# Optimization experiments

Measured on AMD Instinct MI355X. Metric: run time of the kernel, lower is better.

## Reference

```python
import jax, jax.numpy as jnp
import numpy as np

N, E = 50000, 500000
IN_C, HID, OUT_C, HEADS, NL = 128, 16, 16, 8, 4
EPS = 1e-5
NEG_SLOPE = 0.2


def _gatv2(x, src, dst, Wl, Wr, att, bias, concat):
    # GATv2Conv (PyG semantics, eval mode): lin_l on source, lin_r on target,
    # e = a . LeakyReLU(xl[src] + xr[dst]); segment softmax over dst; scatter-sum.
    n = x.shape[0]
    H, C = att.shape
    xl = (x @ Wl).reshape(n, H, C)
    xr = (x @ Wr).reshape(n, H, C)
    e = jax.nn.leaky_relu(xl[src] + xr[dst], NEG_SLOPE)          # [E', H, C]
    logit = jnp.einsum('ehc,hc->eh', e, att)                      # [E', H]
    mx = jax.lax.stop_gradient(jax.ops.segment_max(logit, dst, num_segments=n))
    a = jnp.exp(logit - mx[dst])
    denom = jax.ops.segment_sum(a, dst, num_segments=n)
    alpha = a / denom[dst]                                        # [E', H]
    out = jax.ops.segment_sum(xl[src] * alpha[..., None], dst, num_segments=n)
    out = out.reshape(n, H * C) if concat else out.mean(axis=1)
    return out + bias


def _bn_eval(x, g, b, m, v):
    return (x - m) * jax.lax.rsqrt(v + EPS) * g + b


def setup_inputs() -> dict:
    key = jax.random.key(0)
    ks = jax.random.split(key, 32)
    d = {}
    d['x'] = jax.random.normal(ks[0], (N, IN_C), dtype=jnp.float32)
    d['edge_index'] = jax.random.randint(ks[1], (2, E), 0, N, dtype=jnp.int64)
    HC = HID * HEADS  # 128
    dims_in = [IN_C, HC, HC, HC]
    dims_h = [HEADS, HEADS, HEADS, 1]
    dims_c = [HID, HID, HID, OUT_C]
    ki = 2
    for i in range(NL):
        fan = dims_in[i]
        s = 1.0 / np.sqrt(fan)
        d[f'W{i}l'] = jax.random.uniform(ks[ki], (fan, dims_h[i] * dims_c[i]), minval=-s, maxval=s, dtype=jnp.float32); ki += 1
        d[f'W{i}r'] = jax.random.uniform(ks[ki], (fan, dims_h[i] * dims_c[i]), minval=-s, maxval=s, dtype=jnp.float32); ki += 1
        d[f'a{i}'] = jax.random.normal(ks[ki], (dims_h[i], dims_c[i]), dtype=jnp.float32) * 0.1; ki += 1
        out_dim = dims_h[i] * dims_c[i] if i < NL - 1 else dims_c[i]
        d[f'b{i}'] = jnp.zeros((out_dim,), dtype=jnp.float32)
    for i in range(NL - 1):
        d[f'g{i}'] = jnp.ones((HC,), dtype=jnp.float32) + 0.1 * jax.random.normal(ks[ki], (HC,), dtype=jnp.float32); ki += 1
        d[f'be{i}'] = 0.1 * jax.random.normal(ks[ki], (HC,), dtype=jnp.float32); ki += 1
        d[f'm{i}'] = 0.1 * jax.random.normal(ks[ki], (HC,), dtype=jnp.float32); ki += 1
        d[f'v{i}'] = jnp.ones((HC,), dtype=jnp.float32)
    return d


def reference(x, edge_index, W0l, W0r, a0, b0, W1l, W1r, a1, b1, W2l, W2r, a2, b2, W3l, W3r, a3, b3, g0, be0, m0, v0, g1, be1, m1, v1, g2, be2, m2, v2):
    n = x.shape[0]
    loop = jnp.arange(n, dtype=edge_index.dtype)
    src = jnp.concatenate([edge_index[0], loop])  # add_self_loops=True (PyG default)
    dst = jnp.concatenate([edge_index[1], loop])
    Ws = [(W0l, W0r, a0, b0), (W1l, W1r, a1, b1), (W2l, W2r, a2, b2), (W3l, W3r, a3, b3)]
    bns = [(g0, be0, m0, v0), (g1, be1, m1, v1), (g2, be2, m2, v2)]
    h = x
    for i in range(NL):
        Wl, Wr, att, bias = Ws[i]
        h = _gatv2(h, src, dst, Wl, Wr, att, bias, concat=(i < NL - 1))
        if i < NL - 1:
            g, b, m, v = bns[i]
            h = jax.nn.elu(_bn_eval(h, g, b, m, v))
    return h
```

## Files before the change

### kernel.cpp

```cpp
#include <hip/hip_runtime.h>
#include <hip/hip_fp16.h>
#include <math.h>

static constexpr float BN_EPS = 1e-5f;
static constexpr float NEG = 0.2f;

typedef float f32x4 __attribute__((ext_vector_type(4)));
typedef _Float16 h16x2 __attribute__((ext_vector_type(2)));
typedef _Float16 h16x8 __attribute__((ext_vector_type(8)));


__global__ __launch_bounds__(256) void hist_pack(
    const int* __restrict__ ei, int E, int n, int* __restrict__ cnt,
    const float* __restrict__ W0l, const float* __restrict__ W0r,
    const float* __restrict__ W1l, const float* __restrict__ W1r,
    const float* __restrict__ W2l, const float* __restrict__ W2r,
    const float* __restrict__ W3l, const float* __restrict__ W3r,
    __half* __restrict__ pk0, __half* __restrict__ pk1,
    __half* __restrict__ pk2, __half* __restrict__ pk3,
    const float* __restrict__ b0, const float* __restrict__ b1,
    const float* __restrict__ b2,
    const float* __restrict__ g0, const float* __restrict__ g1,
    const float* __restrict__ g2,
    const float* __restrict__ be0, const float* __restrict__ be1,
    const float* __restrict__ be2,
    const float* __restrict__ m0, const float* __restrict__ m1,
    const float* __restrict__ m2,
    const float* __restrict__ v0, const float* __restrict__ v1,
    const float* __restrict__ v2,
    float* __restrict__ bnA, float* __restrict__ bnB) {
    int b = blockIdx.x;
    if (b < 200) {
        if (threadIdx.x >= 64) return;
        const float *Wl, *Wr;
        __half* packed;
        int tile, NTT, M;
        if (b < 192) {
            int layer = b >> 6;
            tile = b & 63;
            NTT = 16; M = 128;
            Wl = (layer == 0) ? W0l : (layer == 1) ? W1l : W2l;
            Wr = (layer == 0) ? W0r : (layer == 1) ? W1r : W2r;
            packed = (layer == 0) ? pk0 : (layer == 1) ? pk1 : pk2;
        } else {
            tile = b - 192;
            NTT = 2; M = 16;
            Wl = W3l; Wr = W3r; packed = pk3;
        }
        int NT = NTT >> 1;
        int gnt = tile % NTT;
        int kt = tile / NTT;
        int l = threadIdx.x;
        const float* W = (gnt < NT) ? Wl : Wr;
        int col = (gnt % NT) * 16 + (l & 15);
        int krow = kt * 32 + ((l >> 4) << 3);
        size_t base = (size_t)tile * 512 + (size_t)l * 8;
#pragma unroll
        for (int j = 0; j < 8; j++)
            packed[base + j] = __float2half(W[(size_t)(krow + j) * M + col]);
    } else if (b == 200) {
        for (int t = threadIdx.x; t < 384; t += 256) {
            int layer = t >> 7;
            int c = t & 127;
            const float* gg = (layer == 0) ? g0 : (layer == 1) ? g1 : g2;
            const float* ee = (layer == 0) ? be0 : (layer == 1) ? be1 : be2;
            const float* mm = (layer == 0) ? m0 : (layer == 1) ? m1 : m2;
            const float* vv = (layer == 0) ? v0 : (layer == 1) ? v1 : v2;
            const float* bb = (layer == 0) ? b0 : (layer == 1) ? b1 : b2;
            float A = gg[c] * rsqrtf(vv[c] + BN_EPS);
            bnA[t] = A;
            bnB[t] = fmaf(bb[c] - mm[c], A, ee[c]);
        }
    } else {
        int e = (b - 201) * 256 + threadIdx.x;
        int ET = E + n;
        if (e >= ET) return;
        int d = (e < E) ? ei[E + e] : (e - E);
        atomicAdd(&cnt[d], 1);
    }
}


__device__ __forceinline__ void scan_block_body256(
    const int* __restrict__ cnt, int* __restrict__ rowptr,
    int* __restrict__ bsums, int n, int bid, int* s) {
    int t = threadIdx.x;
    int base = bid * 1024 + t * 4;
    int v0 = 0, v1 = 0, v2 = 0, v3 = 0;
    if (base + 3 < n) {
        v0 = cnt[base];     v1 = cnt[base + 1];
        v2 = cnt[base + 2]; v3 = cnt[base + 3];
    } else {
        if (base < n)     v0 = cnt[base];
        if (base + 1 < n) v1 = cnt[base + 1];
        if (base + 2 < n) v2 = cnt[base + 2];
        if (base + 3 < n) v3 = cnt[base + 3];
    }
    int p1 = v0 + v1, p2 = p1 + v2, p3 = p2 + v3;
    s[t] = p3;
    __syncthreads();
    for (int d = 1; d < 256; d <<= 1) {
        int tt = (t >= d) ? s[t - d] : 0;
        __syncthreads();
        s[t] += tt;
        __syncthreads();
    }
    int ex = s[t] - p3;
    if (base < n)     rowptr[base + 1] = ex + v0;
    if (base + 1 < n) rowptr[base + 2] = ex + p1;
    if (base + 2 < n) rowptr[base + 3] = ex + p2;
    if (base + 3 < n) rowptr[base + 4] = ex + p3;
    if (t == 255) bsums[bid] = s[255];
}

__global__ __launch_bounds__(1024) void scan_add2(
    int* __restrict__ rowptr, const int* __restrict__ bsums, int n, int nb,
    int* __restrict__ fill) {
    __shared__ int sex;
    if (threadIdx.x < 64) {
        int L = threadIdx.x;
        int v = (L < nb) ? bsums[L] : 0;
#pragma unroll
        for (int d = 1; d < 64; d <<= 1) {
            int t = __shfl_up(v, d);
            if (L >= d) v += t;
        }
        int ex = __shfl_up(v, 1);
        if (L == 0) ex = 0;
        if (L == (int)blockIdx.x) sex = ex;
    }
    __syncthreads();
    int i = blockIdx.x * 1024 + threadIdx.x;
    if (i < n) {
        int fin = rowptr[i + 1] + sex;
        rowptr[i + 1] = fin;
        if (i + 1 < n) fill[i + 1] = fin;
    }
    if (i == 0) { rowptr[0] = 0; fill[0] = 0; }
}

__global__ void scatter_kernel(const int* __restrict__ ei, int E, int n,
                               int* __restrict__ fill, int* __restrict__ col) {
    int e = blockIdx.x * blockDim.x + threadIdx.x;
    int ET = E + n;
    if (e >= ET) return;
    int s, d;
    if (e < E) { s = ei[e]; d = ei[E + e]; } else { s = e - E; d = s; }
    int pos = atomicAdd(&fill[d], 1);
    col[pos] = s;
}


template <bool FIRST>
__device__ __forceinline__ void gemm_body(
    const __half* __restrict__ xh, const float* __restrict__ xf,
    const __half* __restrict__ packed,
    __half* __restrict__ Y1, __half* __restrict__ Y2, int n, int bid,
    _Float16* sA) {
    const int t = threadIdx.x;
    const int row0 = bid * 64;

    for (int c = t; c < 1024; c += 256) {
        int row = c >> 4;
        int off = (c & 15) * 8;
        int gr = row0 + row;
        if (gr >= n) gr = n - 1;
        if (FIRST) {
            float4 v0 = *(const float4*)&xf[(size_t)gr * 128 + off];
            float4 v1 = *(const float4*)&xf[(size_t)gr * 128 + off + 4];
            h16x8 h = {(_Float16)v0.x, (_Float16)v0.y, (_Float16)v0.z, (_Float16)v0.w,
                       (_Float16)v1.x, (_Float16)v1.y, (_Float16)v1.z, (_Float16)v1.w};
            *(h16x8*)&sA[row * 136 + off] = h;
        } else {
            *(h16x8*)&sA[row * 136 + off] = *(const h16x8*)&xh[(size_t)gr * 128 + off];
        }
    }
    __syncthreads();

    const int lane = t & 63;
    const int s = t >> 6;
    const int lr = lane & 15;
    const int kq = (lane >> 4) * 8;

    h16x8 af[4][4];
#pragma unroll
    for (int rt = 0; rt < 4; rt++)
#pragma unroll
        for (int kt = 0; kt < 4; kt++)
            af[rt][kt] = *(const h16x8*)&sA[(rt * 16 + lr) * 136 + kt * 32 + kq];

    f32x4 acc[4][4];
#pragma unroll
    for (int a = 0; a < 4; a++)
#pragma unroll
        for (int b = 0; b < 4; b++) acc[a][b] = (f32x4){0.f, 0.f, 0.f, 0.f};

#pragma unroll
    for (int kt = 0; kt < 4; kt++) {
#pragma unroll
        for (int ntl = 0; ntl < 4; ntl++) {
            int nt = s * 4 + ntl;
            h16x8 b = *(const h16x8*)&packed[((size_t)(kt * 16 + nt)) * 512 + lane * 8];
#pragma unroll
            for (int rt = 0; rt < 4; rt++)
                acc[ntl][rt] = __builtin_amdgcn_mfma_f32_16x16x32_f16(b, af[rt][kt], acc[ntl][rt], 0, 0, 0);
        }
    }

    __half* Y = (s < 2) ? Y1 : Y2;
    const int colh = (s & 1) * 64;
    const int rq = (lane >> 4) * 4;
#pragma unroll
    for (int rt = 0; rt < 4; rt++) {
        int row = row0 + rt * 16 + lr;
        if (row >= n) continue;
#pragma unroll
        for (int ntl = 0; ntl < 4; ntl++) {
            int c0 = colh + ntl * 16 + rq;
            ushort4 o = make_ushort4(
                __half_as_ushort(__float2half(acc[ntl][rt][0])),
                __half_as_ushort(__float2half(acc[ntl][rt][1])),
                __half_as_ushort(__float2half(acc[ntl][rt][2])),
                __half_as_ushort(__float2half(acc[ntl][rt][3])));
            *(ushort4*)&Y[(size_t)row * 128 + c0] = o;
        }
    }
}

__global__ __launch_bounds__(256) void gemm_h_big2(
    const __half* __restrict__ xh, const __half* __restrict__ packed,
    __half* __restrict__ Y1, __half* __restrict__ Y2, int n) {
    __shared__ __align__(16) char smem[64 * 136 * 2];
    gemm_body<false>(xh, nullptr, packed, Y1, Y2, n, blockIdx.x, (_Float16*)smem);
}

__global__ __launch_bounds__(256) void scanblk_gemm0(
    const int* __restrict__ cnt, int* __restrict__ rowptr,
    int* __restrict__ bsums, int n, int nscan,
    const float* __restrict__ xf, const __half* __restrict__ packed,
    __half* __restrict__ Y1, __half* __restrict__ Y2) {
    __shared__ __align__(16) char smem[64 * 136 * 2];
    int b = blockIdx.x;
    if (b < nscan) {
        scan_block_body256(cnt, rowptr, bsums, n, b, (int*)smem);
    } else {
        gemm_body<true>(nullptr, xf, packed, Y1, Y2, n, b - nscan,
                        (_Float16*)smem);
    }
}


__global__ __launch_bounds__(256) void gemm_h_small(
    const __half* __restrict__ xh, const __half* __restrict__ packed,
    float* __restrict__ Y1, float* __restrict__ Y2, int n) {
    int lane = threadIdx.x & 63;
    int wv = blockIdx.x * 4 + (threadIdx.x >> 6);
    int row0 = wv * 16;
    if (row0 >= n) return;
    int r = row0 + (lane & 15);
    int rl = (r >= n) ? (n - 1) : r;
    int kq = (lane >> 4) * 8;

    h16x8 af[4];
#pragma unroll
    for (int kt = 0; kt < 4; kt++)
        af[kt] = *(const h16x8*)&xh[(size_t)rl * 128 + kt * 32 + kq];

    f32x4 acc[2];
    acc[0] = (f32x4){0.f, 0.f, 0.f, 0.f};
    acc[1] = (f32x4){0.f, 0.f, 0.f, 0.f};

#pragma unroll
    for (int kt = 0; kt < 4; kt++) {
#pragma unroll
        for (int nt = 0; nt < 2; nt++) {
            h16x8 b = *(const h16x8*)&packed[((size_t)(kt * 2 + nt)) * 512 + lane * 8];
            acc[nt] = __builtin_amdgcn_mfma_f32_16x16x32_f16(b, af[kt], acc[nt], 0, 0, 0);
        }
    }

    if (r < n) {
        int rq = (lane >> 4) * 4;
#pragma unroll
        for (int nt = 0; nt < 2; nt++) {
            float* Y = (nt == 0) ? Y1 : Y2;
            *(float4*)&Y[(size_t)r * 16 + rq] =
                make_float4(acc[nt][0], acc[nt][1], acc[nt][2], acc[nt][3]);
        }
    }
}


__device__ __forceinline__ float dot8_h(const h16x2* lp, const h16x2* ap) {
#if __has_builtin(__builtin_amdgcn_fdot2)
    float part = __builtin_amdgcn_fdot2(lp[0], ap[0], 0.f, false);
    part = __builtin_amdgcn_fdot2(lp[1], ap[1], part, false);
    part = __builtin_amdgcn_fdot2(lp[2], ap[2], part, false);
    return __builtin_amdgcn_fdot2(lp[3], ap[3], part, false);
#else
    float part = 0.f;
#pragma unroll
    for (int i = 0; i < 4; i++)
        part += (float)lp[i].x * (float)ap[i].x + (float)lp[i].y * (float)ap[i].y;
    return part;
#endif
}

__global__ __launch_bounds__(256) void agg_h(
    const __half* __restrict__ xl, const __half* __restrict__ xr,
    const int* __restrict__ rowptr, const int* __restrict__ col,
    const float* __restrict__ att,
    const float* __restrict__ bnA, const float* __restrict__ bnB,
    __half* __restrict__ oh, int n) {
    int v = (blockIdx.x * blockDim.x + threadIdx.x) >> 4;
    if (v >= n) return;
    int L = threadIdx.x & 15;
    int ch = L * 8;

    int beg = rowptr[v];
    int end = rowptr[v + 1];
    int cb = beg;
    int cidx = (cb + L < end) ? col[cb + L] : v;

    h16x8 rx = *(const h16x8*)&xr[((size_t)v << 7) + ch];
    float4 av0 = *(const float4*)&att[ch];
    float4 av1 = *(const float4*)&att[ch + 4];
    h16x2 a[4] = {{(_Float16)av0.x, (_Float16)av0.y},
                  {(_Float16)av0.z, (_Float16)av0.w},
                  {(_Float16)av1.x, (_Float16)av1.y},
                  {(_Float16)av1.z, (_Float16)av1.w}};
    const h16x8 neg8 = {(_Float16)NEG, (_Float16)NEG, (_Float16)NEG, (_Float16)NEG,
                        (_Float16)NEG, (_Float16)NEG, (_Float16)NEG, (_Float16)NEG};

    float lrun = 0.f;
    float acc[8] = {0.f, 0.f, 0.f, 0.f, 0.f, 0.f, 0.f, 0.f};

    auto proc = [&](h16x8 hv, bool ok) {
        h16x8 s = hv + rx;
        h16x8 l = __builtin_elementwise_max(s, s * neg8);
        const h16x2* lp = (const h16x2*)&l;
        float part = dot8_h(lp, a);
        part += __shfl_xor(part, 1);
        float p = ok ? __expf(part) : 0.f;
        lrun += p;
        const _Float16* hp = (const _Float16*)&hv;
#pragma unroll
        for (int k = 0; k < 8; k++) acc[k] = fmaf(p, (float)hp[k], acc[k]);
    };

    while (true) {
        int ce = min(end, cb + 16);
        for (int e = cb; e < ce; e += 4) {
            int off = e - cb;
            h16x8 hv[4];
#pragma unroll
            for (int j = 0; j < 4; j++) {
                int u = __shfl(cidx, off + j, 16);
                hv[j] = *(const h16x8*)&xl[((size_t)u << 7) + ch];
            }
#pragma unroll
            for (int j = 0; j < 4; j++) proc(hv[j], e + j < end);
        }
        cb += 16;
        if (cb >= end) break;
        cidx = (cb + L < end) ? col[cb + L] : v;
    }

    float inv = 1.0f / lrun;
    float4 A0 = *(const float4*)&bnA[ch];
    float4 A1 = *(const float4*)&bnA[ch + 4];
    float4 B0 = *(const float4*)&bnB[ch];
    float4 B1 = *(const float4*)&bnB[ch + 4];
    float Av[8] = {A0.x, A0.y, A0.z, A0.w, A1.x, A1.y, A1.z, A1.w};
    float Bv[8] = {B0.x, B0.y, B0.z, B0.w, B1.x, B1.y, B1.z, B1.w};
    h16x8 outv;
#pragma unroll
    for (int k = 0; k < 8; k++) {
        float o = fmaf(acc[k], inv * Av[k], Bv[k]);
        o = o > 0.f ? o : expm1f(o);
        outv[k] = (_Float16)o;
    }
    *(h16x8*)&oh[((size_t)v << 7) + ch] = outv;
}


__global__ __launch_bounds__(256) void agg_f(
    const float* __restrict__ xl, const float* __restrict__ xr,
    const int* __restrict__ rowptr, const int* __restrict__ col,
    const float* __restrict__ att, const float* __restrict__ bias,
    float* __restrict__ out, int n) {
    int v = (blockIdx.x * blockDim.x + threadIdx.x) >> 2;
    if (v >= n) return;
    int L = threadIdx.x & 3;
    int ch = 4 * L;

    int beg = rowptr[v];
    int end = rowptr[v + 1];
    int cb = beg;
    int cidx = (cb + L < end) ? col[cb + L] : v;

    float4 xrv = *(const float4*)&xr[((size_t)v << 4) + ch];
    float4 av = *(const float4*)&att[ch];

    float lrun = 0.f;
    float4 acc = make_float4(0.f, 0.f, 0.f, 0.f);

    while (true) {
        float4 xv[4];
#pragma unroll
        for (int j = 0; j < 4; j++) {
            int u = __shfl(cidx, j, 4);
            xv[j] = *(const float4*)&xl[((size_t)u << 4) + ch];
        }
#pragma unroll
        for (int j = 0; j < 4; j++) {
            bool ok = (cb + j < end);
            float s0 = xv[j].x + xrv.x; s0 = s0 > 0.f ? s0 : NEG * s0;
            float s1 = xv[j].y + xrv.y; s1 = s1 > 0.f ? s1 : NEG * s1;
            float s2 = xv[j].z + xrv.z; s2 = s2 > 0.f ? s2 : NEG * s2;
            float s3 = xv[j].w + xrv.w; s3 = s3 > 0.f ? s3 : NEG * s3;
            float part = fmaf(s0, av.x, fmaf(s1, av.y, fmaf(s2, av.z, s3 * av.w)));
            part += __shfl_xor(part, 1);
            part += __shfl_xor(part, 2);
            float p = ok ? __expf(part) : 0.f;
            lrun += p;
            acc.x = fmaf(p, xv[j].x, acc.x);
            acc.y = fmaf(p, xv[j].y, acc.y);
            acc.z = fmaf(p, xv[j].z, acc.z);
            acc.w = fmaf(p, xv[j].w, acc.w);
        }
        cb += 4;
        if (cb >= end) break;
        cidx = (cb + L < end) ? col[cb + L] : v;
    }

    float inv = 1.0f / lrun;
    float4 b4 = *(const float4*)&bias[ch];
    *(float4*)&out[((size_t)v << 4) + ch] =
        make_float4(fmaf(acc.x, inv, b4.x), fmaf(acc.y, inv, b4.y),
                    fmaf(acc.z, inv, b4.z), fmaf(acc.w, inv, b4.w));
}


extern "C" void kernel_launch(void* const* d_in, const int* in_sizes, int n_in,
                              void* d_out, int out_size, void* d_ws, size_t ws_size,
                              hipStream_t stream) {
    const float* x = (const float*)d_in[0];
    const int* ei = (const int*)d_in[1];
    const float* Wl[4] = {(const float*)d_in[2], (const float*)d_in[6],
                          (const float*)d_in[10], (const float*)d_in[14]};
    const float* Wr[4] = {(const float*)d_in[3], (const float*)d_in[7],
                          (const float*)d_in[11], (const float*)d_in[15]};
    const float* att[4] = {(const float*)d_in[4], (const float*)d_in[8],
                           (const float*)d_in[12], (const float*)d_in[16]};
    const float* bias[4] = {(const float*)d_in[5], (const float*)d_in[9],
                            (const float*)d_in[13], (const float*)d_in[17]};
    const float* g[3] = {(const float*)d_in[18], (const float*)d_in[22], (const float*)d_in[26]};
    const float* be[3] = {(const float*)d_in[19], (const float*)d_in[23], (const float*)d_in[27]};
    const float* bm[3] = {(const float*)d_in[20], (const float*)d_in[24], (const float*)d_in[28]};
    const float* bv[3] = {(const float*)d_in[21], (const float*)d_in[25], (const float*)d_in[29]};

    const int n = in_sizes[0] / 128;
    const int E = in_sizes[1] / 2;
    const int ET = E + n;

    char* p = (char*)d_ws;
    __half* xh = (__half*)p;           p += (size_t)n * 128 * 2;
    __half* xlh = (__half*)p;          p += (size_t)n * 128 * 2;
    __half* xrh = (__half*)p;          p += (size_t)n * 128 * 2;
    float* xl3 = (float*)p;            p += (size_t)n * 16 * 4;
    float* xr3 = (float*)p;            p += (size_t)n * 16 * 4;
    int* rowptr = (int*)p;            p += (size_t)(n + 4) * 4;
    int* cnt = (int*)p;               p += (size_t)n * 4;
    int* fill = (int*)p;              p += (size_t)n * 4;
    int* col = (int*)p;               p += (size_t)ET * 4;
    int* bsums = (int*)p;             p += 256;
    __half* pk[4];
    for (int i = 0; i < 3; i++) { pk[i] = (__half*)p; p += 4 * 16 * 512 * 2; }
    pk[3] = (__half*)p;               p += 4 * 2 * 512 * 2;
    float* bnA = (float*)p;           p += 384 * 4;
    float* bnB = (float*)p;           p += 384 * 4;

    (void)hipMemsetAsync(cnt, 0, (size_t)n * 4, stream);

    const int tb = 256;
    const int histBlocks = (ET + tb - 1) / tb;
    hist_pack<<<201 + histBlocks, tb, 0, stream>>>(
        ei, E, n, cnt,
        Wl[0], Wr[0], Wl[1], Wr[1], Wl[2], Wr[2], Wl[3], Wr[3],
        pk[0], pk[1], pk[2], pk[3],
        bias[0], bias[1], bias[2],
        g[0], g[1], g[2], be[0], be[1], be[2],
        bm[0], bm[1], bm[2], bv[0], bv[1], bv[2],
        bnA, bnB);

    const int nb = (n + 1023) / 1024;
    const int gb64 = (n + 63) / 64;
    const int gemmBlocksSmall = ((n + 15) / 16 + 3) / 4;
    const int aggBlocksH = (n + 15) / 16;
    const int aggBlocksF = (n + 63) / 64;

    scanblk_gemm0<<<nb + gb64, 256, 0, stream>>>(
        cnt, rowptr, bsums, n, nb, x, pk[0], xlh, xrh);
    scan_add2<<<nb, 1024, 0, stream>>>(rowptr, bsums, n, nb, fill);
    scatter_kernel<<<(ET + tb - 1) / tb, tb, 0, stream>>>(ei, E, n, fill, col);

    agg_h<<<aggBlocksH, 256, 0, stream>>>(
        xlh, xrh, rowptr, col, att[0], bnA, bnB, xh, n);
    for (int i = 1; i < 3; i++) {
        gemm_h_big2<<<gb64, 256, 0, stream>>>(xh, pk[i], xlh, xrh, n);
        agg_h<<<aggBlocksH, 256, 0, stream>>>(
            xlh, xrh, rowptr, col, att[i], bnA + 128 * i, bnB + 128 * i, xh, n);
    }
    gemm_h_small<<<gemmBlocksSmall, 256, 0, stream>>>(xh, pk[3], xl3, xr3, n);
    agg_f<<<aggBlocksF, 256, 0, stream>>>(
        xl3, xr3, rowptr, col, att[3], bias[3], (float*)d_out, n);
}
```

Baseline: 331.1 us.

## Process aggregation nodes in degree-sorted order to balance wavefront work

```diff
diff --git a/kernel.cpp b/kernel.cpp
--- a/kernel.cpp
+++ b/kernel.cpp
@@ -115,9 +115,11 @@
 
 __global__ __launch_bounds__(1024) void scan_add2(
     int* __restrict__ rowptr, const int* __restrict__ bsums, int n, int nb,
-    int* __restrict__ fill) {
+    int* __restrict__ fill, const int* __restrict__ cnt, int* __restrict__ dbin) {
     __shared__ int sex;
+    __shared__ int hb[64];
     if (threadIdx.x < 64) {
+        hb[threadIdx.x] = 0;
         int L = threadIdx.x;
         int v = (L < nb) ? bsums[L] : 0;
 #pragma unroll
@@ -135,19 +137,52 @@
         int fin = rowptr[i + 1] + sex;
         rowptr[i + 1] = fin;
         if (i + 1 < n) fill[i + 1] = fin;
+        int deg = cnt[i];
+        atomicAdd(&hb[deg < 63 ? deg : 63], 1);
     }
     if (i == 0) { rowptr[0] = 0; fill[0] = 0; }
-}
-
-__global__ void scatter_kernel(const int* __restrict__ ei, int E, int n,
-                               int* __restrict__ fill, int* __restrict__ col) {
-    int e = blockIdx.x * blockDim.x + threadIdx.x;
-    int ET = E + n;
-    if (e >= ET) return;
-    int s, d;
-    if (e < E) { s = ei[e]; d = ei[E + e]; } else { s = e - E; d = s; }
-    int pos = atomicAdd(&fill[d], 1);
-    col[pos] = s;
+    __syncthreads();
+    if (threadIdx.x < 64 && hb[threadIdx.x])
+        atomicAdd(&dbin[threadIdx.x], hb[threadIdx.x]);
+}
+
+__global__ __launch_bounds__(256) void scatter_kernel(
+    const int* __restrict__ ei, int E, int n,
+    int* __restrict__ fill, int* __restrict__ col, int edgeBlocks,
+    const int* __restrict__ cnt, const int* __restrict__ dbin,
+    int* __restrict__ dfill, int* __restrict__ perm) {
+    int b = blockIdx.x;
+    if (b < edgeBlocks) {
+        int e = b * 256 + threadIdx.x;
+        int ET = E + n;
+        if (e >= ET) return;
+        int s, d;
+        if (e < E) { s = ei[e]; d = ei[E + e]; } else { s = e - E; d = s; }
+        int pos = atomicAdd(&fill[d], 1);
+        col[pos] = s;
+    } else {
+        __shared__ int sstart[64];
+        if (threadIdx.x < 64) {
+            int L = threadIdx.x;
+            int v = dbin[L];
+#pragma unroll
+            for (int d = 1; d < 64; d <<= 1) {
+                int t = __shfl_up(v, d);
+                if (L >= d) v += t;
+            }
+            int ex = __shfl_up(v, 1);
+            if (L == 0) ex = 0;
+            sstart[L] = ex;
+        }
+        __syncthreads();
+        int v = (b - edgeBlocks) * 256 + threadIdx.x;
+        if (v < n) {
+            int deg = cnt[v];
+            int bin = deg < 63 ? deg : 63;
+            int pos = sstart[bin] + atomicAdd(&dfill[bin], 1);
+            perm[pos] = v;
+        }
+    }
 }
 
 
@@ -309,11 +344,13 @@
 __global__ __launch_bounds__(256) void agg_h(
     const __half* __restrict__ xl, const __half* __restrict__ xr,
     const int* __restrict__ rowptr, const int* __restrict__ col,
+    const int* __restrict__ perm,
     const float* __restrict__ att,
     const float* __restrict__ bnA, const float* __restrict__ bnB,
     __half* __restrict__ oh, int n) {
-    int v = (blockIdx.x * blockDim.x + threadIdx.x) >> 4;
-    if (v >= n) return;
+    int g = (blockIdx.x * blockDim.x + threadIdx.x) >> 4;
+    if (g >= n) return;
+    int v = perm[g];
     int L = threadIdx.x & 15;
     int ch = L * 8;
 
@@ -387,10 +424,12 @@
 __global__ __launch_bounds__(256) void agg_f(
     const float* __restrict__ xl, const float* __restrict__ xr,
     const int* __restrict__ rowptr, const int* __restrict__ col,
+    const int* __restrict__ perm,
     const float* __restrict__ att, const float* __restrict__ bias,
     float* __restrict__ out, int n) {
-    int v = (blockIdx.x * blockDim.x + threadIdx.x) >> 2;
-    if (v >= n) return;
+    int g = (blockIdx.x * blockDim.x + threadIdx.x) >> 2;
+    if (g >= n) return;
+    int v = perm[g];
     int L = threadIdx.x & 3;
     int ch = 4 * L;
 
@@ -472,7 +511,10 @@
     float* xr3 = (float*)p;            p += (size_t)n * 16 * 4;
     int* rowptr = (int*)p;            p += (size_t)(n + 4) * 4;
     int* cnt = (int*)p;               p += (size_t)n * 4;
+    int* dbin = (int*)p;              p += 256;
+    int* dfill = (int*)p;             p += 256;
     int* fill = (int*)p;              p += (size_t)n * 4;
+    int* perm = (int*)p;              p += (size_t)n * 4;
     int* col = (int*)p;               p += (size_t)ET * 4;
     int* bsums = (int*)p;             p += 256;
     __half* pk[4];
@@ -481,7 +523,7 @@
     float* bnA = (float*)p;           p += 384 * 4;
     float* bnB = (float*)p;           p += 384 * 4;
 
-    (void)hipMemsetAsync(cnt, 0, (size_t)n * 4, stream);
+    (void)hipMemsetAsync(cnt, 0, (size_t)n * 4 + 512, stream);
 
     const int tb = 256;
     const int histBlocks = (ET + tb - 1) / tb;
@@ -499,20 +541,22 @@
     const int gemmBlocksSmall = ((n + 15) / 16 + 3) / 4;
     const int aggBlocksH = (n + 15) / 16;
     const int aggBlocksF = (n + 63) / 64;
+    const int nodeBlocks = (n + tb - 1) / tb;
 
     scanblk_gemm0<<<nb + gb64, 256, 0, stream>>>(
         cnt, rowptr, bsums, n, nb, x, pk[0], xlh, xrh);
-    scan_add2<<<nb, 1024, 0, stream>>>(rowptr, bsums, n, nb, fill);
-    scatter_kernel<<<(ET + tb - 1) / tb, tb, 0, stream>>>(ei, E, n, fill, col);
+    scan_add2<<<nb, 1024, 0, stream>>>(rowptr, bsums, n, nb, fill, cnt, dbin);
+    scatter_kernel<<<histBlocks + nodeBlocks, tb, 0, stream>>>(
+        ei, E, n, fill, col, histBlocks, cnt, dbin, dfill, perm);
 
     agg_h<<<aggBlocksH, 256, 0, stream>>>(
-        xlh, xrh, rowptr, col, att[0], bnA, bnB, xh, n);
+        xlh, xrh, rowptr, col, perm, att[0], bnA, bnB, xh, n);
     for (int i = 1; i < 3; i++) {
         gemm_h_big2<<<gb64, 256, 0, stream>>>(xh, pk[i], xlh, xrh, n);
         agg_h<<<aggBlocksH, 256, 0, stream>>>(
-            xlh, xrh, rowptr, col, att[i], bnA + 128 * i, bnB + 128 * i, xh, n);
+            xlh, xrh, rowptr, col, perm, att[i], bnA + 128 * i, bnB + 128 * i, xh, n);
     }
     gemm_h_small<<<gemmBlocksSmall, 256, 0, stream>>>(xh, pk[3], xl3, xr3, n);
     agg_f<<<aggBlocksF, 256, 0, stream>>>(
-        xl3, xr3, rowptr, col, att[3], bias[3], (float*)d_out, n);
-}
+        xl3, xr3, rowptr, col, perm, att[3], bias[3], (float*)d_out, n);
+}
```

Result: slower. 485.8 us (+46.7%).

## Fuse scan finalization with edge scatter and widen aggregation gather batch

Applied to the files above, without the earlier changes.

```diff
diff --git a/kernel.cpp b/kernel.cpp
--- a/kernel.cpp
+++ b/kernel.cpp
@@ -113,41 +113,44 @@
     if (t == 255) bsums[bid] = s[255];
 }
 
-__global__ __launch_bounds__(1024) void scan_add2(
-    int* __restrict__ rowptr, const int* __restrict__ bsums, int n, int nb,
-    int* __restrict__ fill) {
-    __shared__ int sex;
+__global__ __launch_bounds__(256) void scatfin(
+    const int* __restrict__ ei, int E, int n,
+    const int* __restrict__ rowraw, const int* __restrict__ bsums, int nb,
+    int* __restrict__ fill, int* __restrict__ col, int* __restrict__ rowfin,
+    int nbF) {
+    __shared__ int spre[64];
     if (threadIdx.x < 64) {
         int L = threadIdx.x;
-        int v = (L < nb) ? bsums[L] : 0;
+        int bv = (L < nb) ? bsums[L] : 0;
 #pragma unroll
         for (int d = 1; d < 64; d <<= 1) {
-            int t = __shfl_up(v, d);
-            if (L >= d) v += t;
-        }
-        int ex = __shfl_up(v, 1);
+            int t = __shfl_up(bv, d);
+            if (L >= d) bv += t;
+        }
+        int ex = __shfl_up(bv, 1);
         if (L == 0) ex = 0;
-        if (L == (int)blockIdx.x) sex = ex;
+        spre[L] = ex;
     }
     __syncthreads();
-    int i = blockIdx.x * 1024 + threadIdx.x;
-    if (i < n) {
-        int fin = rowptr[i + 1] + sex;
-        rowptr[i + 1] = fin;
-        if (i + 1 < n) fill[i + 1] = fin;
-    }
-    if (i == 0) { rowptr[0] = 0; fill[0] = 0; }
-}
-
-__global__ void scatter_kernel(const int* __restrict__ ei, int E, int n,
-                               int* __restrict__ fill, int* __restrict__ col) {
-    int e = blockIdx.x * blockDim.x + threadIdx.x;
-    int ET = E + n;
-    if (e >= ET) return;
-    int s, d;
-    if (e < E) { s = ei[e]; d = ei[E + e]; } else { s = e - E; d = s; }
-    int pos = atomicAdd(&fill[d], 1);
-    col[pos] = s;
+    int b = blockIdx.x;
+    if (b < nbF) {
+        int i0 = b * 1024 + threadIdx.x * 4;
+#pragma unroll
+        for (int j = 0; j < 4; j++) {
+            int i = i0 + j;
+            if (i < n) rowfin[i + 1] = rowraw[i + 1] + spre[i >> 10];
+        }
+        if (b == 0 && threadIdx.x == 0) rowfin[0] = 0;
+    } else {
+        int e = (b - nbF) * 256 + threadIdx.x;
+        int ET = E + n;
+        if (e >= ET) return;
+        int s, d;
+        if (e < E) { s = ei[e]; d = ei[E + e]; } else { s = e - E; d = s; }
+        int pos = atomicAdd(&fill[d], 1);
+        int base = (d == 0) ? 0 : (rowraw[d] + spre[(d - 1) >> 10]);
+        col[base + pos] = s;
+    }
 }
 
 
@@ -235,14 +238,14 @@
 }
 
 __global__ __launch_bounds__(256) void scanblk_gemm0(
-    const int* __restrict__ cnt, int* __restrict__ rowptr,
+    const int* __restrict__ cnt, int* __restrict__ rowraw,
     int* __restrict__ bsums, int n, int nscan,
     const float* __restrict__ xf, const __half* __restrict__ packed,
     __half* __restrict__ Y1, __half* __restrict__ Y2) {
     __shared__ __align__(16) char smem[64 * 136 * 2];
     int b = blockIdx.x;
     if (b < nscan) {
-        scan_block_body256(cnt, rowptr, bsums, n, b, (int*)smem);
+        scan_block_body256(cnt, rowraw, bsums, n, b, (int*)smem);
     } else {
         gemm_body<true>(nullptr, xf, packed, Y1, Y2, n, b - nscan,
                         (_Float16*)smem);
@@ -350,16 +353,16 @@
 
     while (true) {
         int ce = min(end, cb + 16);
-        for (int e = cb; e < ce; e += 4) {
+        for (int e = cb; e < ce; e += 8) {
             int off = e - cb;
-            h16x8 hv[4];
-#pragma unroll
-            for (int j = 0; j < 4; j++) {
+            h16x8 hv[8];
+#pragma unroll
+            for (int j = 0; j < 8; j++) {
                 int u = __shfl(cidx, off + j, 16);
                 hv[j] = *(const h16x8*)&xl[((size_t)u << 7) + ch];
             }
 #pragma unroll
-            for (int j = 0; j < 4; j++) proc(hv[j], e + j < end);
+            for (int j = 0; j < 8; j++) proc(hv[j], e + j < end);
         }
         cb += 16;
         if (cb >= end) break;
@@ -470,7 +473,8 @@
     __half* xrh = (__half*)p;          p += (size_t)n * 128 * 2;
     float* xl3 = (float*)p;            p += (size_t)n * 16 * 4;
     float* xr3 = (float*)p;            p += (size_t)n * 16 * 4;
-    int* rowptr = (int*)p;            p += (size_t)(n + 4) * 4;
+    int* rowraw = (int*)p;            p += (size_t)(n + 4) * 4;
+    int* rowfin = (int*)p;            p += (size_t)(n + 4) * 4;
     int* cnt = (int*)p;               p += (size_t)n * 4;
     int* fill = (int*)p;              p += (size_t)n * 4;
     int* col = (int*)p;               p += (size_t)ET * 4;
@@ -481,7 +485,7 @@
     float* bnA = (float*)p;           p += 384 * 4;
     float* bnB = (float*)p;           p += 384 * 4;
 
-    (void)hipMemsetAsync(cnt, 0, (size_t)n * 4, stream);
+    (void)hipMemsetAsync(cnt, 0, (size_t)n * 8, stream);
 
     const int tb = 256;
     const int histBlocks = (ET + tb - 1) / tb;
@@ -501,18 +505,18 @@
     const int aggBlocksF = (n + 63) / 64;
 
     scanblk_gemm0<<<nb + gb64, 256, 0, stream>>>(
-        cnt, rowptr, bsums, n, nb, x, pk[0], xlh, xrh);
-    scan_add2<<<nb, 1024, 0, stream>>>(rowptr, bsums, n, nb, fill);
-    scatter_kernel<<<(ET + tb - 1) / tb, tb, 0, stream>>>(ei, E, n, fill, col);
+        cnt, rowraw, bsums, n, nb, x, pk[0], xlh, xrh);
+    scatfin<<<nb + histBlocks, tb, 0, stream>>>(
+        ei, E, n, rowraw, bsums, nb, fill, col, rowfin, nb);
 
     agg_h<<<aggBlocksH, 256, 0, stream>>>(
-        xlh, xrh, rowptr, col, att[0], bnA, bnB, xh, n);
+        xlh, xrh, rowfin, col, att[0], bnA, bnB, xh, n);
     for (int i = 1; i < 3; i++) {
         gemm_h_big2<<<gb64, 256, 0, stream>>>(xh, pk[i], xlh, xrh, n);
         agg_h<<<aggBlocksH, 256, 0, stream>>>(
-            xlh, xrh, rowptr, col, att[i], bnA + 128 * i, bnB + 128 * i, xh, n);
+            xlh, xrh, rowfin, col, att[i], bnA + 128 * i, bnB + 128 * i, xh, n);
     }
     gemm_h_small<<<gemmBlocksSmall, 256, 0, stream>>>(xh, pk[3], xl3, xr3, n);
     agg_f<<<aggBlocksF, 256, 0, stream>>>(
-        xl3, xr3, rowptr, col, att[3], bias[3], (float*)d_out, n);
-}
+        xl3, xr3, rowfin, col, att[3], bias[3], (float*)d_out, n);
+}
```

Result: no change. 331.4 us, median of 2 (+0.1%).
